# Optimization experiments

Measured on AMD Instinct MI355X. Metric: run time of the kernel, lower is better.

## Reference

```python
import jax, jax.numpy as jnp
import numpy as np

B, N, D, H, QV = 8, 1024, 64, 4, 32
C = 2 * D + 1          # combined_dim = 129
K = C // 8             # per-head qk dim = 16
M_PER = 512
M = B * M_PER
NEG = -9e15


def setup_inputs() -> dict:
    key = jax.random.key(0)
    ks = jax.random.split(key, 24)
    s = 0.05
    x = jax.random.normal(ks[0], (B, N, D + 1), jnp.float32)
    h = jax.random.normal(ks[1], (B, N, D), jnp.float32)
    query_vectors = jax.random.normal(ks[2], (M, QV), jnp.float32)
    adj = jax.random.randint(ks[3], (N, N), 0, 2, jnp.int32)
    # unique observed nodes per graph (mimics torch.where on an obs mask)
    perm = jax.vmap(lambda k: jax.random.permutation(k, N))(jax.random.split(ks[4], B))
    nodes_n = perm[:, :M_PER].reshape(-1).astype(jnp.int32)
    nodes_b = jnp.repeat(jnp.arange(B, dtype=jnp.int32), M_PER)
    # per-head attention projections, stacked over heads
    Wq = jax.random.normal(ks[5], (H, C, K), jnp.float32) * s
    bq = jax.random.normal(ks[6], (H, K), jnp.float32) * s
    Wk = jax.random.normal(ks[7], (H, C, K), jnp.float32) * s
    bk = jax.random.normal(ks[8], (H, K), jnp.float32) * s
    Wv = jax.random.normal(ks[9], (H, C, C), jnp.float32) * s
    bv = jax.random.normal(ks[10], (H, C), jnp.float32) * s
    # attentionMLP: Linear(H*C, C) -> ReLU -> Linear(C, C)
    W1 = jax.random.normal(ks[11], (H * C, C), jnp.float32) * s
    b1 = jax.random.normal(ks[12], (C,), jnp.float32) * s
    W2 = jax.random.normal(ks[13], (C, C), jnp.float32) * s
    b2 = jax.random.normal(ks[14], (C,), jnp.float32) * s
    # MLP_Param hypernetwork tensors: W[qvd, in=C, out=D], b[qvd, D]
    Wr = jax.random.normal(ks[15], (QV, C, D), jnp.float32) * s
    br = jax.random.normal(ks[16], (QV, D), jnp.float32) * s
    Wu = jax.random.normal(ks[17], (QV, C, D), jnp.float32) * s
    bu = jax.random.normal(ks[18], (QV, D), jnp.float32) * s
    Wc = jax.random.normal(ks[19], (QV, C, D), jnp.float32) * s
    bc = jax.random.normal(ks[20], (QV, D), jnp.float32) * s
    return dict(x=x, h=h, query_vectors=query_vectors, adj=adj,
                nodes_b=nodes_b, nodes_n=nodes_n,
                Wq=Wq, bq=bq, Wk=Wk, bk=bk, Wv=Wv, bv=bv,
                W1=W1, b1=b1, W2=W2, b2=b2,
                Wr=Wr, br=br, Wu=Wu, bu=bu, Wc=Wc, bc=bc)


def _mlp_param(sel, qv, W, b):
    # hypernetwork: per-node generated linear layer
    Wn = jnp.einsum('md,dio->mio', qv, W)   # [M, C, D]
    bn = qv @ b                              # [M, D]
    return jnp.einsum('mi,mio->mo', sel, Wn) + bn


def reference(x, h, query_vectors, adj, nodes_b, nodes_n,
              Wq, bq, Wk, bk, Wv, bv, W1, b1, W2, b2,
              Wr, br, Wu, bu, Wc, bc):
    combined = jnp.concatenate([x, h], axis=-1)                      # [B,N,C]
    q = jnp.einsum('bnc,hck->hbnk', combined, Wq) + bq[:, None, None, :]
    k = jnp.einsum('bnc,hck->hbnk', combined, Wk) + bk[:, None, None, :]
    v = jnp.einsum('bnc,hcd->hbnd', combined, Wv) + bv[:, None, None, :]
    scores = jnp.einsum('hbnk,hbmk->hbnm', q, k) / jnp.sqrt(jnp.float32(K))
    scores = jax.nn.leaky_relu(scores, 0.2)
    scores = jnp.where(adj == 0, NEG, scores)                        # [N,N] broadcast
    attn = jax.nn.softmax(scores, axis=-1)                           # [H,B,N,N]
    hp = jnp.einsum('hbnm,hbmd->hbnd', attn, v)                      # [H,B,N,C]
    # permute(1,2,0,3).reshape -> concat heads per node
    attn_cat = jnp.transpose(hp, (1, 2, 0, 3)).reshape(B, N, H * C)
    mlp_out = jax.nn.relu(attn_cat @ W1 + b1) @ W2 + b2              # [B,N,C]
    combined = mlp_out + combined                                    # skip connection
    sel = combined[nodes_b, nodes_n]                                 # [M,C]
    r = jax.nn.sigmoid(_mlp_param(sel, query_vectors, Wr, br))       # [M,D]
    u = jax.nn.sigmoid(_mlp_param(sel, query_vectors, Wu, bu))       # [M,D]
    h = h.at[nodes_b, nodes_n].set(r * h[nodes_b, nodes_n])
    combined_new = jnp.concatenate([x, h], axis=-1)
    cand = jnp.tanh(_mlp_param(combined_new[nodes_b, nodes_n], query_vectors, Wc, bc))
    new_h = (1.0 - u) * h[nodes_b, nodes_n] + u * cand               # [M,D]
    return new_h
```

## Files before the change

### kernel.cpp

```cpp
#include <hip/hip_runtime.h>

#define DEVINL __device__ __forceinline__

typedef unsigned short ushort_t;
typedef unsigned long long u64;
typedef __attribute__((ext_vector_type(8))) short short8;
typedef __attribute__((ext_vector_type(8))) unsigned short ushort8;
typedef __attribute__((ext_vector_type(4))) float f32x4;

constexpr int B_ = 8, N_ = 1024, D_ = 64, H_ = 4, QV_ = 32;
constexpr int C_ = 129, K_ = 16, M_ = 4096;
constexpr int CP = 132;
constexpr int NG = B_ * N_;
constexpr int CBS = 160;
constexpr int VTN = 144;
constexpr int KT = 4256;
constexpr int NKT = 133;
constexpr int HPS = 544;

constexpr size_t o_cb    = 0;
constexpr size_t o_qb    = o_cb  + (size_t)NG * CBS / 2;
constexpr size_t o_kb    = o_qb  + (size_t)H_ * NG * 16 / 2;
constexpr size_t o_adjb  = o_kb  + (size_t)H_ * NG * 16 / 2;
constexpr size_t o_wqk   = o_adjb + 32768;
constexpr size_t o_wvt   = o_wqk + (size_t)H_ * 32 * CBS / 2;
constexpr size_t o_vT    = o_wvt + (size_t)H_ * VTN * CBS / 2;
constexpr size_t o_hpb   = o_vT  + (size_t)H_ * VTN * NG / 2;
constexpr size_t o_cpost = o_hpb + (size_t)M_ * HPS / 2;
constexpr size_t o_W1T   = o_cpost + (size_t)M_ * CP;
constexpr size_t o_W2T   = o_W1T + (size_t)144 * HPS / 2;
constexpr size_t o_wtru  = o_W2T + (size_t)144 * 160 / 2;
constexpr size_t o_wtc   = o_wtru + (size_t)128 * KT / 2;
constexpr size_t o_A     = o_wtc + (size_t)64 * KT / 2;
constexpr size_t o_pru   = o_A + (size_t)M_ * KT / 2;
constexpr size_t o_pc2   = o_pru + (size_t)4 * M_ * 128;
constexpr size_t o_cin   = o_vT;

constexpr int SEG0 = NG * CBS;
constexpr int SEG1 = SEG0 + H_ * 32 * CBS;
constexpr int SEG2 = SEG1 + H_ * VTN * CBS;
constexpr int SEG3 = SEG2 + 144 * HPS;
constexpr int SEG4 = SEG3 + 144 * 160;
constexpr int SEG5 = SEG4 + 192 * KT;
constexpr int SEG6 = SEG5 + 1024 * 16 * 64;

DEVINL float4 ld4(const float* p) { return *reinterpret_cast<const float4*>(p); }
DEVINL void st4(float* p, float4 v) { *reinterpret_cast<float4*>(p) = v; }
DEVINL ushort_t f2bf(float f) {
    unsigned int u = __float_as_uint(f);
    u += 0x7FFFu + ((u >> 16) & 1u);
    return (ushort_t)(u >> 16);
}

__global__ void k_prep(const float* __restrict__ x, const float* __restrict__ h,
                       const float* __restrict__ Wq, const float* __restrict__ bq,
                       const float* __restrict__ Wk, const float* __restrict__ bk,
                       const float* __restrict__ Wv, const float* __restrict__ bv,
                       const float* __restrict__ W1, const float* __restrict__ W2,
                       const float* __restrict__ Wr, const float* __restrict__ br,
                       const float* __restrict__ Wu, const float* __restrict__ bu,
                       const float* __restrict__ Wc, const float* __restrict__ bc,
                       const int* __restrict__ adj,
                       ushort_t* __restrict__ cb, ushort_t* __restrict__ wqk,
                       ushort_t* __restrict__ wvt, ushort_t* __restrict__ W1T,
                       ushort_t* __restrict__ W2T, ushort_t* __restrict__ wtru,
                       ushort_t* __restrict__ wtc, u64* __restrict__ ab) {
    int idx = blockIdx.x * 256 + threadIdx.x;
    if (idx < SEG0) {
        int g = idx / CBS, kk = idx - g * CBS;
        float v;
        if (kk < 65) v = x[g * 65 + kk];
        else if (kk < 129) v = h[g * 64 + (kk - 65)];
        else if (kk == 129) v = 1.0f;
        else v = 0.f;
        cb[idx] = f2bf(v);
    } else if (idx < SEG1) {
        int j = idx - SEG0;
        int hh = j / (32 * CBS); int rem = j - hh * 32 * CBS;
        int o = rem / CBS, kk = rem - o * CBS;
        float v = 0.f;
        if (o < 16) {
            if (kk < 129) v = Wq[(size_t)(hh * C_ + kk) * K_ + o];
            else if (kk == 129) v = bq[hh * K_ + o];
        } else {
            int o2 = o - 16;
            if (kk < 129) v = Wk[(size_t)(hh * C_ + kk) * K_ + o2];
            else if (kk == 129) v = bk[hh * K_ + o2];
        }
        wqk[j] = f2bf(v);
    } else if (idx < SEG2) {
        int j = idx - SEG1;
        int hh = j / (VTN * CBS); int rem = j - hh * VTN * CBS;
        int n = rem / CBS, kk = rem - n * CBS;
        float v = 0.f;
        if (n < C_) {
            if (kk < 129) v = Wv[(size_t)(hh * C_ + kk) * C_ + n];
            else if (kk == 129) v = bv[hh * C_ + n];
        }
        wvt[j] = f2bf(v);
    } else if (idx < SEG3) {
        int j = idx - SEG2;
        int o = j / HPS, k = j - o * HPS;
        float v = (o < C_ && k < 516) ? W1[(size_t)k * C_ + o] : 0.f;
        W1T[j] = f2bf(v);
    } else if (idx < SEG4) {
        int j = idx - SEG3;
        int o = j / 160, k = j - o * 160;
        float v = (o < C_ && k < C_) ? W2[(size_t)k * C_ + o] : 0.f;
        W2T[j] = f2bf(v);
    } else if (idx < SEG5) {
        int j = idx - SEG4;
        int row = j / KT, k = j - row * KT;
        float v;
        if (k >= 4224) {
            int d = k - 4224;
            if (row < 64) v = br[d * 64 + row];
            else if (row < 128) v = bu[d * 64 + row - 64];
            else v = bc[d * 64 + row - 128];
        } else {
            int d = k / 132, i = k - d * 132;
            if (i >= 129) v = 0.f;
            else if (row < 64) v = Wr[(size_t)(d * 129 + i) * 64 + row];
            else if (row < 128) v = Wu[(size_t)(d * 129 + i) * 64 + row - 64];
            else v = Wc[(size_t)(d * 129 + i) * 64 + row - 128];
        }
        int kt = k >> 5, kj = k & 31;
        if (row < 128) wtru[((size_t)kt * 128 + row) * 32 + kj] = f2bf(v);
        else wtc[((size_t)kt * 64 + (row - 128)) * 32 + kj] = f2bf(v);
    } else if (idx < SEG6) {
        int j = idx - SEG5;
        int word = j >> 6, lane = j & 63;
        int row = word >> 4, wj = word & 15;
        u64 m = __ballot(adj[(size_t)row * N_ + wj * 64 + lane] != 0);
        if (lane == 0) ab[word] = m;
    }
}

__global__ __launch_bounds__(256) void k_qkv(
    const ushort_t* __restrict__ cb, const ushort_t* __restrict__ wqk,
    const ushort_t* __restrict__ wvt,
    ushort_t* __restrict__ qbo, ushort_t* __restrict__ kbo, ushort_t* __restrict__ vTg) {
    const int t = threadIdx.x;
    const int g0 = blockIdx.x * 16;
    const int hh = blockIdx.y;
    const int lane = t & 63, w = t >> 6;
    const int am = lane & 15, aq = lane >> 4;
    short8 cbf[5];
    const ushort_t* Cr = cb + (size_t)(g0 + am) * CBS + aq * 8;
#pragma unroll
    for (int kt = 0; kt < 5; ++kt)
        cbf[kt] = *reinterpret_cast<const short8*>(Cr + kt * 32);
#pragma unroll
    for (int s = 0; s < 3; ++s) {
        int u = w + 4 * s;
        if (u >= 11) break;
        f32x4 acc = f32x4{0.f, 0.f, 0.f, 0.f};
        if (u < 2) {
            const ushort_t* Bp = wqk + ((size_t)(hh * 32 + u * 16 + am)) * CBS + aq * 8;
#pragma unroll
            for (int kt = 0; kt < 5; ++kt)
                acc = __builtin_amdgcn_mfma_f32_16x16x32_bf16(
                    cbf[kt], *reinterpret_cast<const short8*>(Bp + kt * 32), acc, 0, 0, 0);
            ushort_t* dst = u ? kbo : qbo;
#pragma unroll
            for (int i = 0; i < 4; ++i)
                dst[(size_t)(hh * NG + g0 + aq * 4 + i) * 16 + am] = f2bf(acc[i]);
        } else {
            int vt = u - 2;
            const ushort_t* Ap = wvt + ((size_t)(hh * VTN + vt * 16 + am)) * CBS + aq * 8;
#pragma unroll
            for (int kt = 0; kt < 5; ++kt)
                acc = __builtin_amdgcn_mfma_f32_16x16x32_bf16(
                    *reinterpret_cast<const short8*>(Ap + kt * 32), cbf[kt], acc, 0, 0, 0);
#pragma unroll
            for (int i = 0; i < 4; ++i)
                vTg[(size_t)(hh * VTN + vt * 16 + aq * 4 + i) * NG + g0 + am] = f2bf(acc[i]);
        }
    }
}

__global__ __launch_bounds__(256) void k_attn(
    const ushort_t* __restrict__ qb, const ushort_t* __restrict__ kb,
    const ushort_t* __restrict__ vTg, const u64* __restrict__ adjb,
    const int* __restrict__ nodes_b, const int* __restrict__ nodes_n,
    ushort_t* __restrict__ hpb) {
    __shared__ u64 Msk[16][16];
    __shared__ alignas(16) ushort_t Pb[4][16 * 72];
    __shared__ float Ored[3][16 * 144];
    __shared__ float Lpart[4][16];
    __shared__ float Linv[16];
    __shared__ int Nrow[16];
    const int t = threadIdx.x;
    const int bi = blockIdx.x;
    const int mx = ((bi & 7) << 5) + (bi >> 3);
    const int m0 = mx * 16;
    const int hh = blockIdx.y;
    const int b = nodes_b[m0];
    if (t < 16) Nrow[t] = nodes_n[m0 + t];
    __syncthreads();
    { int r = t >> 4, wj = t & 15; Msk[r][wj] = adjb[Nrow[r] * 16 + wj]; }
    const int lane = t & 63, w = t >> 6;
    const int am = lane & 15, aq = lane >> 4;
    short8 qf = short8{0, 0, 0, 0, 0, 0, 0, 0};
    if (aq < 2)
        qf = *reinterpret_cast<const short8*>(&qb[(size_t)(hh * NG + b * N_ + Nrow[am]) * 16 + aq * 8]);
    __syncthreads();
    ushort_t* Pw = Pb[w];
    const ushort_t* kbase = kb + ((size_t)hh * NG + b * N_) * 16;
    f32x4 accv[9];
#pragma unroll
    for (int j = 0; j < 9; ++j) accv[j] = f32x4{0.f, 0.f, 0.f, 0.f};
    float lsum[4] = {0.f, 0.f, 0.f, 0.f};

    for (int ti = 0; ti < 4; ++ti) {
        const int tile = w + 4 * ti;
        const int c0 = tile * 64;
        u64 mrow[4];
#pragma unroll
        for (int i = 0; i < 4; ++i) mrow[i] = Msk[aq * 4 + i][tile];
#pragma unroll
        for (int nt = 0; nt < 4; ++nt) {
            int col = c0 + nt * 16 + am;
            short8 bf = short8{0, 0, 0, 0, 0, 0, 0, 0};
            if (aq < 2)
                bf = *reinterpret_cast<const short8*>(&kbase[(size_t)col * 16 + aq * 8]);
            f32x4 sv = __builtin_amdgcn_mfma_f32_16x16x32_bf16(qf, bf, f32x4{0.f, 0.f, 0.f, 0.f}, 0, 0, 0);
#pragma unroll
            for (int i = 0; i < 4; ++i) {
                float s = sv[i] * 0.25f;
                s = (s >= 0.f) ? s : 0.2f * s;
                float p = ((mrow[i] >> (nt * 16 + am)) & 1ull) ? __expf(s) : 0.f;
                lsum[i] += p;
                Pw[(aq * 4 + i) * 72 + nt * 16 + am] = f2bf(p);
            }
        }
#pragma unroll
        for (int kh = 0; kh < 2; ++kh) {
            short8 af = *reinterpret_cast<const short8*>(&Pw[am * 72 + kh * 32 + aq * 8]);
#pragma unroll
            for (int nt = 0; nt < 9; ++nt) {
                short8 bfr = *reinterpret_cast<const short8*>(
                    &vTg[(size_t)(hh * VTN + nt * 16 + am) * NG + b * N_ + c0 + kh * 32 + aq * 8]);
                accv[nt] = __builtin_amdgcn_mfma_f32_16x16x32_bf16(af, bfr, accv[nt], 0, 0, 0);
            }
        }
    }
#pragma unroll
    for (int i = 0; i < 4; ++i) {
        float v = lsum[i];
        v += __shfl_xor(v, 1); v += __shfl_xor(v, 2);
        v += __shfl_xor(v, 4); v += __shfl_xor(v, 8);
        if (am == 0) Lpart[w][aq * 4 + i] = v;
    }
    if (w > 0) {
#pragma unroll
        for (int nt = 0; nt < 9; ++nt)
#pragma unroll
            for (int i = 0; i < 4; ++i)
                Ored[w - 1][(aq * 4 + i) * 144 + nt * 16 + am] = accv[nt][i];
    }
    __syncthreads();
    if (w == 0) {
        if (t < 16) {
            float s = Lpart[0][t] + Lpart[1][t] + Lpart[2][t] + Lpart[3][t];
            Linv[t] = (s > 0.f) ? 1.f / s : 0.f;
        }
#pragma unroll
        for (int nt = 0; nt < 9; ++nt) {
            int col = nt * 16 + am;
            if (col < C_) {
#pragma unroll
                for (int i = 0; i < 4; ++i) {
                    int row = aq * 4 + i;
                    float val = accv[nt][i] + Ored[0][row * 144 + col]
                              + Ored[1][row * 144 + col] + Ored[2][row * 144 + col];
                    hpb[(size_t)(m0 + row) * HPS + hh * C_ + col] = f2bf(val * Linv[row]);
                }
            }
        }
    }
    if (hh == 3) {
        for (int idx = t; idx < 16 * 28; idx += 256) {
            int rr = idx / 28, cc = 516 + (idx - rr * 28);
            hpb[(size_t)(m0 + rr) * HPS + cc] = 0;
        }
    }
}

__global__ __launch_bounds__(256) void k_mlp(
    const ushort_t* __restrict__ hpb,
    const ushort_t* __restrict__ W1T, const float* __restrict__ b1,
    const ushort_t* __restrict__ W2T, const float* __restrict__ b2,
    const float* __restrict__ x, const float* __restrict__ h,
    const int* __restrict__ nb, const int* __restrict__ nn,
    float* __restrict__ cpost) {
    __shared__ alignas(16) ushort_t Hs[16 * 168];
    const int t = threadIdx.x;
    const int m0 = blockIdx.x * 16;
    const int lane = t & 63, w = t >> 6;
    const int am = lane & 15, aq = lane >> 4;
    f32x4 acc[3];
#pragma unroll
    for (int j = 0; j < 3; ++j) acc[j] = f32x4{0.f, 0.f, 0.f, 0.f};
    const ushort_t* Ar = hpb + (size_t)(m0 + am) * HPS;
    for (int kt = 0; kt < 17; ++kt) {
        short8 af = *reinterpret_cast<const short8*>(Ar + kt * 32 + aq * 8);
#pragma unroll
        for (int j = 0; j < 3; ++j) {
            int nt = w + 4 * j;
            if (nt < 9) {
                short8 bf = *reinterpret_cast<const short8*>(W1T + (size_t)(nt * 16 + am) * HPS + kt * 32 + aq * 8);
                acc[j] = __builtin_amdgcn_mfma_f32_16x16x32_bf16(af, bf, acc[j], 0, 0, 0);
            }
        }
    }
#pragma unroll
    for (int j = 0; j < 3; ++j) {
        int nt = w + 4 * j;
        if (nt < 9) {
            int col = nt * 16 + am;
            float bb = (col < C_) ? b1[col] : 0.f;
#pragma unroll
            for (int i = 0; i < 4; ++i) {
                int row = aq * 4 + i;
                float v = (col < C_) ? fmaxf(acc[j][i] + bb, 0.f) : 0.f;
                Hs[row * 168 + col] = f2bf(v);
            }
        }
    }
    { int row = t >> 4, cc = 144 + (t & 15); Hs[row * 168 + cc] = 0; }
    __syncthreads();
    f32x4 acc2[3];
#pragma unroll
    for (int j = 0; j < 3; ++j) acc2[j] = f32x4{0.f, 0.f, 0.f, 0.f};
    for (int kt = 0; kt < 5; ++kt) {
        short8 af = *reinterpret_cast<const short8*>(&Hs[am * 168 + kt * 32 + aq * 8]);
#pragma unroll
        for (int j = 0; j < 3; ++j) {
            int nt = w + 4 * j;
            if (nt < 9) {
                short8 bf = *reinterpret_cast<const short8*>(W2T + (size_t)(nt * 16 + am) * 160 + kt * 32 + aq * 8);
                acc2[j] = __builtin_amdgcn_mfma_f32_16x16x32_bf16(af, bf, acc2[j], 0, 0, 0);
            }
        }
    }
#pragma unroll
    for (int j = 0; j < 3; ++j) {
        int nt = w + 4 * j;
        if (nt < 9) {
            int col = nt * 16 + am;
            if (col < C_) {
                float bb = b2[col];
#pragma unroll
                for (int i = 0; i < 4; ++i) {
                    int m = m0 + aq * 4 + i;
                    int b = nb[m], n = nn[m];
                    float sk = (col < 65) ? x[(b * N_ + n) * 65 + col]
                                          : h[(b * N_ + n) * D_ + (col - 65)];
                    cpost[(size_t)m * CP + col] = acc2[j][i] + bb + sk;
                }
            }
        }
    }
    if (t < 48) {
        int rr = t / 3, cc = 129 + (t - (t / 3) * 3);
        cpost[(size_t)(m0 + rr) * CP + cc] = 0.f;
    }
}

__global__ __launch_bounds__(256) void k_arow(const float* __restrict__ src,
                                              const float* __restrict__ qv,
                                              ushort_t* __restrict__ A) {
    __shared__ float sq[CP];
    __shared__ float qs[QV_];
    const int t = threadIdx.x;
    const int m = blockIdx.x;
    if (t < CP) sq[t] = src[(size_t)m * CP + t];
    if (t >= 224) qs[t - 224] = qv[m * QV_ + (t - 224)];
    __syncthreads();
    for (int k = t; k < 4224; k += 256) {
        int d = k / 132, i = k - d * 132;
        A[((size_t)(k >> 5) * M_ + m) * 32 + (k & 31)] = f2bf(qs[d] * sq[i]);
    }
    if (t < QV_) A[((size_t)132 * M_ + m) * 32 + t] = f2bf(qs[t]);
}

template<int NN>
__global__ __launch_bounds__(256) void k_gemm(const ushort_t* __restrict__ A,
                                              const ushort_t* __restrict__ WT,
                                              float* __restrict__ part) {
    const int t = threadIdx.x;
    const int m0 = blockIdx.x * 32;
    const int z = blockIdx.y;
    const int lane = t & 63, w = t >> 6;
    const int am = lane & 15, aq = lane >> 4;
    constexpr int NTpW = NN / 64;
    const int ktb = z * 34;
    const int kte = (ktb + 34 < NKT) ? ktb + 34 : NKT;
    f32x4 acc[2][NTpW];
#pragma unroll
    for (int r2 = 0; r2 < 2; ++r2)
#pragma unroll
        for (int j = 0; j < NTpW; ++j) acc[r2][j] = f32x4{0.f, 0.f, 0.f, 0.f};
    for (int kt = ktb; kt < kte; ++kt) {
        const ushort_t* Ab = A + ((size_t)kt * M_ + m0) * 32 + aq * 8;
        short8 a0 = *reinterpret_cast<const short8*>(Ab + am * 32);
        short8 a1 = *reinterpret_cast<const short8*>(Ab + (am + 16) * 32);
        const ushort_t* Bb = WT + (size_t)kt * NN * 32 + am * 32 + aq * 8;
#pragma unroll
        for (int j = 0; j < NTpW; ++j) {
            int nt = w + 4 * j;
            short8 bf = *reinterpret_cast<const short8*>(Bb + nt * 16 * 32);
            acc[0][j] = __builtin_amdgcn_mfma_f32_16x16x32_bf16(a0, bf, acc[0][j], 0, 0, 0);
            acc[1][j] = __builtin_amdgcn_mfma_f32_16x16x32_bf16(a1, bf, acc[1][j], 0, 0, 0);
        }
    }
#pragma unroll
    for (int j = 0; j < NTpW; ++j) {
        int n = (w + 4 * j) * 16 + am;
#pragma unroll
        for (int r2 = 0; r2 < 2; ++r2)
#pragma unroll
            for (int i = 0; i < 4; ++i) {
                int m = m0 + r2 * 16 + aq * 4 + i;
                part[((size_t)z * M_ + m) * NN + n] = acc[r2][j][i];
            }
    }
}

__global__ void k_build_cin(const float* __restrict__ x, const float* __restrict__ h,
                            const int* __restrict__ nb, const int* __restrict__ nn,
                            const float* __restrict__ pru, float* __restrict__ cin) {
    int idx = blockIdx.x * 256 + threadIdx.x;
    if (idx >= M_ * CP) return;
    int m = idx / CP, i = idx - m * CP;
    int b = nb[m], n = nn[m];
    float val;
    if (i < 65) val = x[(b * N_ + n) * 65 + i];
    else if (i < C_) {
        int o = i - 65;
        const size_t S = (size_t)M_ * 128;
        size_t base = (size_t)m * 128 + o;
        float s = pru[base] + pru[S + base] + pru[2 * S + base] + pru[3 * S + base];
        float rv = 1.f / (1.f + __expf(-s));
        val = rv * h[(b * N_ + n) * D_ + o];
    } else val = 0.f;
    cin[idx] = val;
}

__global__ void k_final(const float* __restrict__ pru, const float* __restrict__ pc,
                        const float* __restrict__ cin, float* __restrict__ out) {
    int idx = blockIdx.x * 256 + threadIdx.x;
    if (idx >= M_ * D_) return;
    int m = idx >> 6, o = idx & 63;
    const size_t Su = (size_t)M_ * 128;
    size_t bu = (size_t)m * 128 + 64 + o;
    float su = pru[bu] + pru[Su + bu] + pru[2 * Su + bu] + pru[3 * Su + bu];
    float uv = 1.f / (1.f + __expf(-su));
    const size_t Sc = (size_t)M_ * 64;
    size_t bc = (size_t)m * 64 + o;
    float sc = pc[bc] + pc[Sc + bc] + pc[2 * Sc + bc] + pc[3 * Sc + bc];
    float cand = tanhf(sc);
    float hn = cin[(size_t)m * CP + 65 + o];
    out[idx] = (1.f - uv) * hn + uv * cand;
}

extern "C" void kernel_launch(void* const* d_in, const int* in_sizes, int n_in,
                              void* d_out, int out_size, void* d_ws, size_t ws_size,
                              hipStream_t stream) {
    const float* x   = (const float*)d_in[0];
    const float* h   = (const float*)d_in[1];
    const float* qv  = (const float*)d_in[2];
    const int*   adj = (const int*)d_in[3];
    const int*   nb  = (const int*)d_in[4];
    const int*   nn  = (const int*)d_in[5];
    const float* Wq  = (const float*)d_in[6];
    const float* bq  = (const float*)d_in[7];
    const float* Wk  = (const float*)d_in[8];
    const float* bk  = (const float*)d_in[9];
    const float* Wv  = (const float*)d_in[10];
    const float* bv  = (const float*)d_in[11];
    const float* W1  = (const float*)d_in[12];
    const float* b1  = (const float*)d_in[13];
    const float* W2  = (const float*)d_in[14];
    const float* b2  = (const float*)d_in[15];
    const float* Wr  = (const float*)d_in[16];
    const float* br  = (const float*)d_in[17];
    const float* Wu  = (const float*)d_in[18];
    const float* bu  = (const float*)d_in[19];
    const float* Wc  = (const float*)d_in[20];
    const float* bc  = (const float*)d_in[21];
    float* ws = (float*)d_ws;
    float* out = (float*)d_out;

    ushort_t* cb   = (ushort_t*)(ws + o_cb);
    ushort_t* qb   = (ushort_t*)(ws + o_qb);
    ushort_t* kb   = (ushort_t*)(ws + o_kb);
    u64*      ab   = (u64*)(ws + o_adjb);
    ushort_t* wqk  = (ushort_t*)(ws + o_wqk);
    ushort_t* wvt  = (ushort_t*)(ws + o_wvt);
    ushort_t* vTg  = (ushort_t*)(ws + o_vT);
    ushort_t* hpb  = (ushort_t*)(ws + o_hpb);
    float* cpost = ws + o_cpost;
    ushort_t* W1T  = (ushort_t*)(ws + o_W1T);
    ushort_t* W2T  = (ushort_t*)(ws + o_W2T);
    ushort_t* wtru = (ushort_t*)(ws + o_wtru);
    ushort_t* wtc  = (ushort_t*)(ws + o_wtc);
    ushort_t* Abuf = (ushort_t*)(ws + o_A);
    float* pru   = ws + o_pru;
    float* pc    = ws + o_pc2;
    float* cin   = ws + o_cin;

    k_prep<<<(SEG6 + 255) / 256, 256, 0, stream>>>(
        x, h, Wq, bq, Wk, bk, Wv, bv, W1, W2, Wr, br, Wu, bu, Wc, bc, adj,
        cb, wqk, wvt, W1T, W2T, wtru, wtc, ab);
    k_qkv<<<dim3(NG / 16, H_), 256, 0, stream>>>(cb, wqk, wvt, qb, kb, vTg);
    k_attn<<<dim3(M_ / 16, H_), 256, 0, stream>>>(qb, kb, vTg, ab, nb, nn, hpb);
    k_mlp<<<M_ / 16, 256, 0, stream>>>(hpb, W1T, b1, W2T, b2, x, h, nb, nn, cpost);
    k_arow<<<M_, 256, 0, stream>>>(cpost, qv, Abuf);
    k_gemm<128><<<dim3(M_ / 32, 4), 256, 0, stream>>>(Abuf, wtru, pru);
    k_build_cin<<<(M_ * CP + 255) / 256, 256, 0, stream>>>(x, h, nb, nn, pru, cin);
    k_arow<<<M_, 256, 0, stream>>>(cin, qv, Abuf);
    k_gemm<64><<<dim3(M_ / 32, 4), 256, 0, stream>>>(Abuf, wtc, pc);
    k_final<<<(M_ * D_ + 255) / 256, 256, 0, stream>>>(pru, pc, cin, out);
}
```

Baseline: 266.4 us.

## Tile bf16 operands into k-major 32-wide blocks and fuse cin build into arow

Rewrites the bf16 operand buffers (cb, wqk, wvt, W1T, W2T, hpb) into a k-tile-major layout of 32-element chunks, so the MFMA fragment loads in k_qkv and k_mlp read contiguous rows per k-tile instead of long strided rows. It also removes the k_build_cin kernel and the cin buffer. A new k_arow2 computes the gated input directly from x, h and pru, and k_final recomputes r*h instead of reading cin. This saves one launch and a global round trip, at the cost of recomputing the sigmoid of r in k_final.

```diff
diff --git a/kernel.cpp b/kernel.cpp
--- a/kernel.cpp
+++ b/kernel.cpp
@@ -34,7 +34,6 @@
 constexpr size_t o_A     = o_wtc + (size_t)64 * KT / 2;
 constexpr size_t o_pru   = o_A + (size_t)M_ * KT / 2;
 constexpr size_t o_pc2   = o_pru + (size_t)4 * M_ * 128;
-constexpr size_t o_cin   = o_vT;
 
 constexpr int SEG0 = NG * CBS;
 constexpr int SEG1 = SEG0 + H_ * 32 * CBS;
@@ -73,7 +72,7 @@
         else if (kk < 129) v = h[g * 64 + (kk - 65)];
         else if (kk == 129) v = 1.0f;
         else v = 0.f;
-        cb[idx] = f2bf(v);
+        cb[((size_t)(kk >> 5) * NG + g) * 32 + (kk & 31)] = f2bf(v);
     } else if (idx < SEG1) {
         int j = idx - SEG0;
         int hh = j / (32 * CBS); int rem = j - hh * 32 * CBS;
@@ -87,7 +86,7 @@
             if (kk < 129) v = Wk[(size_t)(hh * C_ + kk) * K_ + o2];
             else if (kk == 129) v = bk[hh * K_ + o2];
         }
-        wqk[j] = f2bf(v);
+        wqk[((size_t)(hh * 5 + (kk >> 5)) * 32 + o) * 32 + (kk & 31)] = f2bf(v);
     } else if (idx < SEG2) {
         int j = idx - SEG1;
         int hh = j / (VTN * CBS); int rem = j - hh * VTN * CBS;
@@ -97,17 +96,17 @@
             if (kk < 129) v = Wv[(size_t)(hh * C_ + kk) * C_ + n];
             else if (kk == 129) v = bv[hh * C_ + n];
         }
-        wvt[j] = f2bf(v);
+        wvt[((size_t)(hh * 5 + (kk >> 5)) * 144 + n) * 32 + (kk & 31)] = f2bf(v);
     } else if (idx < SEG3) {
         int j = idx - SEG2;
         int o = j / HPS, k = j - o * HPS;
         float v = (o < C_ && k < 516) ? W1[(size_t)k * C_ + o] : 0.f;
-        W1T[j] = f2bf(v);
+        W1T[((size_t)(k >> 5) * 144 + o) * 32 + (k & 31)] = f2bf(v);
     } else if (idx < SEG4) {
         int j = idx - SEG3;
         int o = j / 160, k = j - o * 160;
         float v = (o < C_ && k < C_) ? W2[(size_t)k * C_ + o] : 0.f;
-        W2T[j] = f2bf(v);
+        W2T[((size_t)(k >> 5) * 144 + o) * 32 + (k & 31)] = f2bf(v);
     } else if (idx < SEG5) {
         int j = idx - SEG4;
         int row = j / KT, k = j - row * KT;
@@ -146,32 +145,33 @@
     const int lane = t & 63, w = t >> 6;
     const int am = lane & 15, aq = lane >> 4;
     short8 cbf[5];
-    const ushort_t* Cr = cb + (size_t)(g0 + am) * CBS + aq * 8;
 #pragma unroll
     for (int kt = 0; kt < 5; ++kt)
-        cbf[kt] = *reinterpret_cast<const short8*>(Cr + kt * 32);
+        cbf[kt] = *reinterpret_cast<const short8*>(&cb[((size_t)kt * NG + g0 + am) * 32 + aq * 8]);
 #pragma unroll
     for (int s = 0; s < 3; ++s) {
         int u = w + 4 * s;
         if (u >= 11) break;
         f32x4 acc = f32x4{0.f, 0.f, 0.f, 0.f};
         if (u < 2) {
-            const ushort_t* Bp = wqk + ((size_t)(hh * 32 + u * 16 + am)) * CBS + aq * 8;
-#pragma unroll
-            for (int kt = 0; kt < 5; ++kt)
-                acc = __builtin_amdgcn_mfma_f32_16x16x32_bf16(
-                    cbf[kt], *reinterpret_cast<const short8*>(Bp + kt * 32), acc, 0, 0, 0);
+#pragma unroll
+            for (int kt = 0; kt < 5; ++kt) {
+                short8 bf = *reinterpret_cast<const short8*>(
+                    &wqk[((size_t)(hh * 5 + kt) * 32 + u * 16 + am) * 32 + aq * 8]);
+                acc = __builtin_amdgcn_mfma_f32_16x16x32_bf16(cbf[kt], bf, acc, 0, 0, 0);
+            }
             ushort_t* dst = u ? kbo : qbo;
 #pragma unroll
             for (int i = 0; i < 4; ++i)
                 dst[(size_t)(hh * NG + g0 + aq * 4 + i) * 16 + am] = f2bf(acc[i]);
         } else {
             int vt = u - 2;
-            const ushort_t* Ap = wvt + ((size_t)(hh * VTN + vt * 16 + am)) * CBS + aq * 8;
-#pragma unroll
-            for (int kt = 0; kt < 5; ++kt)
-                acc = __builtin_amdgcn_mfma_f32_16x16x32_bf16(
-                    *reinterpret_cast<const short8*>(Ap + kt * 32), cbf[kt], acc, 0, 0, 0);
+#pragma unroll
+            for (int kt = 0; kt < 5; ++kt) {
+                short8 af = *reinterpret_cast<const short8*>(
+                    &wvt[((size_t)(hh * 5 + kt) * 144 + vt * 16 + am) * 32 + aq * 8]);
+                acc = __builtin_amdgcn_mfma_f32_16x16x32_bf16(af, cbf[kt], acc, 0, 0, 0);
+            }
 #pragma unroll
             for (int i = 0; i < 4; ++i)
                 vTg[(size_t)(hh * VTN + vt * 16 + aq * 4 + i) * NG + g0 + am] = f2bf(acc[i]);
@@ -269,12 +269,13 @@
         for (int nt = 0; nt < 9; ++nt) {
             int col = nt * 16 + am;
             if (col < C_) {
+                int k = hh * C_ + col;
 #pragma unroll
                 for (int i = 0; i < 4; ++i) {
                     int row = aq * 4 + i;
                     float val = accv[nt][i] + Ored[0][row * 144 + col]
                               + Ored[1][row * 144 + col] + Ored[2][row * 144 + col];
-                    hpb[(size_t)(m0 + row) * HPS + hh * C_ + col] = f2bf(val * Linv[row]);
+                    hpb[((size_t)(k >> 5) * M_ + m0 + row) * 32 + (k & 31)] = f2bf(val * Linv[row]);
                 }
             }
         }
@@ -282,7 +283,7 @@
     if (hh == 3) {
         for (int idx = t; idx < 16 * 28; idx += 256) {
             int rr = idx / 28, cc = 516 + (idx - rr * 28);
-            hpb[(size_t)(m0 + rr) * HPS + cc] = 0;
+            hpb[((size_t)(cc >> 5) * M_ + m0 + rr) * 32 + (cc & 31)] = 0;
         }
     }
 }
@@ -302,14 +303,14 @@
     f32x4 acc[3];
 #pragma unroll
     for (int j = 0; j < 3; ++j) acc[j] = f32x4{0.f, 0.f, 0.f, 0.f};
-    const ushort_t* Ar = hpb + (size_t)(m0 + am) * HPS;
     for (int kt = 0; kt < 17; ++kt) {
-        short8 af = *reinterpret_cast<const short8*>(Ar + kt * 32 + aq * 8);
+        short8 af = *reinterpret_cast<const short8*>(&hpb[((size_t)kt * M_ + m0 + am) * 32 + aq * 8]);
 #pragma unroll
         for (int j = 0; j < 3; ++j) {
             int nt = w + 4 * j;
             if (nt < 9) {
-                short8 bf = *reinterpret_cast<const short8*>(W1T + (size_t)(nt * 16 + am) * HPS + kt * 32 + aq * 8);
+                short8 bf = *reinterpret_cast<const short8*>(
+                    &W1T[((size_t)kt * 144 + nt * 16 + am) * 32 + aq * 8]);
                 acc[j] = __builtin_amdgcn_mfma_f32_16x16x32_bf16(af, bf, acc[j], 0, 0, 0);
             }
         }
@@ -339,7 +340,8 @@
         for (int j = 0; j < 3; ++j) {
             int nt = w + 4 * j;
             if (nt < 9) {
-                short8 bf = *reinterpret_cast<const short8*>(W2T + (size_t)(nt * 16 + am) * 160 + kt * 32 + aq * 8);
+                short8 bf = *reinterpret_cast<const short8*>(
+                    &W2T[((size_t)kt * 144 + nt * 16 + am) * 32 + aq * 8]);
                 acc2[j] = __builtin_amdgcn_mfma_f32_16x16x32_bf16(af, bf, acc2[j], 0, 0, 0);
             }
         }
@@ -385,6 +387,36 @@
     if (t < QV_) A[((size_t)132 * M_ + m) * 32 + t] = f2bf(qs[t]);
 }
 
+__global__ __launch_bounds__(256) void k_arow2(const float* __restrict__ x,
+                                               const float* __restrict__ h,
+                                               const int* __restrict__ nb,
+                                               const int* __restrict__ nn,
+                                               const float* __restrict__ pru,
+                                               const float* __restrict__ qv,
+                                               ushort_t* __restrict__ A) {
+    __shared__ float sq[CP];
+    __shared__ float qs[QV_];
+    const int t = threadIdx.x;
+    const int m = blockIdx.x;
+    const int b = nb[m], n = nn[m];
+    if (t < 65) sq[t] = x[(b * N_ + n) * 65 + t];
+    else if (t < 129) {
+        int o = t - 65;
+        const size_t S = (size_t)M_ * 128;
+        size_t base = (size_t)m * 128 + o;
+        float s = pru[base] + pru[S + base] + pru[2 * S + base] + pru[3 * S + base];
+        float rv = 1.f / (1.f + __expf(-s));
+        sq[t] = rv * h[(b * N_ + n) * D_ + o];
+    } else if (t < 132) sq[t] = 0.f;
+    if (t >= 224) qs[t - 224] = qv[m * QV_ + (t - 224)];
+    __syncthreads();
+    for (int k = t; k < 4224; k += 256) {
+        int d = k / 132, i = k - d * 132;
+        A[((size_t)(k >> 5) * M_ + m) * 32 + (k & 31)] = f2bf(qs[d] * sq[i]);
+    }
+    if (t < QV_) A[((size_t)132 * M_ + m) * 32 + t] = f2bf(qs[t]);
+}
+
 template<int NN>
 __global__ __launch_bounds__(256) void k_gemm(const ushort_t* __restrict__ A,
                                               const ushort_t* __restrict__ WT,
@@ -428,40 +460,26 @@
     }
 }
 
-__global__ void k_build_cin(const float* __restrict__ x, const float* __restrict__ h,
-                            const int* __restrict__ nb, const int* __restrict__ nn,
-                            const float* __restrict__ pru, float* __restrict__ cin) {
-    int idx = blockIdx.x * 256 + threadIdx.x;
-    if (idx >= M_ * CP) return;
-    int m = idx / CP, i = idx - m * CP;
-    int b = nb[m], n = nn[m];
-    float val;
-    if (i < 65) val = x[(b * N_ + n) * 65 + i];
-    else if (i < C_) {
-        int o = i - 65;
-        const size_t S = (size_t)M_ * 128;
-        size_t base = (size_t)m * 128 + o;
-        float s = pru[base] + pru[S + base] + pru[2 * S + base] + pru[3 * S + base];
-        float rv = 1.f / (1.f + __expf(-s));
-        val = rv * h[(b * N_ + n) * D_ + o];
-    } else val = 0.f;
-    cin[idx] = val;
-}
-
 __global__ void k_final(const float* __restrict__ pru, const float* __restrict__ pc,
-                        const float* __restrict__ cin, float* __restrict__ out) {
+                        const float* __restrict__ h,
+                        const int* __restrict__ nb, const int* __restrict__ nn,
+                        float* __restrict__ out) {
     int idx = blockIdx.x * 256 + threadIdx.x;
     if (idx >= M_ * D_) return;
     int m = idx >> 6, o = idx & 63;
     const size_t Su = (size_t)M_ * 128;
-    size_t bu = (size_t)m * 128 + 64 + o;
+    size_t br_ = (size_t)m * 128 + o;
+    size_t bu = br_ + 64;
+    float sr = pru[br_] + pru[Su + br_] + pru[2 * Su + br_] + pru[3 * Su + br_];
+    float rv = 1.f / (1.f + __expf(-sr));
     float su = pru[bu] + pru[Su + bu] + pru[2 * Su + bu] + pru[3 * Su + bu];
     float uv = 1.f / (1.f + __expf(-su));
     const size_t Sc = (size_t)M_ * 64;
-    size_t bc = (size_t)m * 64 + o;
-    float sc = pc[bc] + pc[Sc + bc] + pc[2 * Sc + bc] + pc[3 * Sc + bc];
+    size_t bcx = (size_t)m * 64 + o;
+    float sc = pc[bcx] + pc[Sc + bcx] + pc[2 * Sc + bcx] + pc[3 * Sc + bcx];
     float cand = tanhf(sc);
-    float hn = cin[(size_t)m * CP + 65 + o];
+    int b = nb[m], n = nn[m];
+    float hn = rv * h[(b * N_ + n) * D_ + o];
     out[idx] = (1.f - uv) * hn + uv * cand;
 }
 
@@ -509,7 +527,6 @@
     ushort_t* Abuf = (ushort_t*)(ws + o_A);
     float* pru   = ws + o_pru;
     float* pc    = ws + o_pc2;
-    float* cin   = ws + o_cin;
 
     k_prep<<<(SEG6 + 255) / 256, 256, 0, stream>>>(
         x, h, Wq, bq, Wk, bk, Wv, bv, W1, W2, Wr, br, Wu, bu, Wc, bc, adj,
@@ -519,8 +536,7 @@
     k_mlp<<<M_ / 16, 256, 0, stream>>>(hpb, W1T, b1, W2T, b2, x, h, nb, nn, cpost);
     k_arow<<<M_, 256, 0, stream>>>(cpost, qv, Abuf);
     k_gemm<128><<<dim3(M_ / 32, 4), 256, 0, stream>>>(Abuf, wtru, pru);
-    k_build_cin<<<(M_ * CP + 255) / 256, 256, 0, stream>>>(x, h, nb, nn, pru, cin);
-    k_arow<<<M_, 256, 0, stream>>>(cin, qv, Abuf);
+    k_arow2<<<M_, 256, 0, stream>>>(x, h, nb, nn, pru, qv, Abuf);
     k_gemm<64><<<dim3(M_ / 32, 4), 256, 0, stream>>>(Abuf, wtc, pc);
-    k_final<<<(M_ * D_ + 255) / 256, 256, 0, stream>>>(pru, pc, cin, out);
-}
+    k_final<<<(M_ * D_ + 255) / 256, 256, 0, stream>>>(pru, pc, h, nb, nn, out);
+}
```

Measured after the change: 262.1 us. No clear change (-1.6%).
